# Performance work log

Measured on AMD Instinct MI355X. Metric: run time of the kernel, lower is better.

The kernel has to match this reference:

```python
import jax, jax.numpy as jnp
import numpy as np

B, S, V, E, H, MAX_OOVS = 32, 1024, 32000, 256, 512, 12
D2 = 2 * H + 100          # encoder feature dim after binary concat
IN = E + D2               # GRU input size


def setup_inputs() -> dict:
    key = jax.random.key(0)
    ks = jax.random.split(key, 18)
    sc = 0.02
    return {
        "input_idx": jax.random.randint(ks[0], (B,), 0, V),
        "encoded": jax.random.normal(ks[1], (B, S, 2 * H), jnp.float32),
        "encoded_idx": jax.random.randint(ks[2], (B, S), 0, V + MAX_OOVS),
        "prev_state": jax.random.normal(ks[3], (B, H), jnp.float32),
        "weighted": jax.random.normal(ks[4], (B, 1, D2), jnp.float32),
        "binary_vectors": jax.random.uniform(ks[5], (B, S, 1), jnp.float32),
        "order": 1,
        "embed_table": jax.random.normal(ks[6], (V, E), jnp.float32) * sc,
        "W_ih": jax.random.normal(ks[7], (3 * H, IN), jnp.float32) * sc,
        "b_ih": jax.random.normal(ks[8], (3 * H,), jnp.float32) * sc,
        "W_hh": jax.random.normal(ks[9], (3 * H, H), jnp.float32) * sc,
        "b_hh": jax.random.normal(ks[10], (3 * H,), jnp.float32) * sc,
        "Wo_w": jax.random.normal(ks[11], (V, H), jnp.float32) * sc,
        "Wo_b": jax.random.normal(ks[12], (V,), jnp.float32) * sc,
        "Wc_w": jax.random.normal(ks[13], (H, D2), jnp.float32) * sc,
        "Wc_b": jax.random.normal(ks[14], (H,), jnp.float32) * sc,
        "Ws_w": jax.random.normal(ks[15], (H, D2), jnp.float32) * sc,
        "Ws_b": jax.random.normal(ks[16], (H,), jnp.float32) * sc,
    }


def _gru_step(x, h, W_ih, b_ih, W_hh, b_hh):
    # torch nn.GRU single-step math
    gi = x @ W_ih.T + b_ih
    gh = h @ W_hh.T + b_hh
    i_r, i_z, i_n = jnp.split(gi, 3, axis=1)
    h_r, h_z, h_n = jnp.split(gh, 3, axis=1)
    r = jax.nn.sigmoid(i_r + h_r)
    z = jax.nn.sigmoid(i_z + h_z)
    n = jnp.tanh(i_n + r * h_n)
    return (1.0 - z) * n + z * h


def reference(input_idx, encoded, encoded_idx, prev_state, weighted,
              binary_vectors, order, embed_table, W_ih, b_ih, W_hh, b_hh,
              Wo_w, Wo_b, Wc_w, Wc_b, Ws_w, Ws_b):
    b, s = encoded.shape[0], encoded.shape[1]
    vocab = Wo_w.shape[0]
    # concat binary feature expanded to 100 channels -> (b, s, 2H+100)
    bin100 = jnp.broadcast_to(binary_vectors, (b, s, 100))
    enc = jnp.concatenate([encoded, bin100], axis=2)

    if order == 0:
        prev_state = enc[:, -1] @ Ws_w.T + Ws_b
        weighted = jnp.zeros((b, 1, enc.shape[2]), enc.dtype)

    emb = embed_table[input_idx][:, None, :]          # (b,1,E)
    x = jnp.concatenate([emb, weighted], axis=2)[:, 0]  # (b, IN)
    state = _gru_step(x, prev_state, W_ih, b_ih, W_hh, b_hh)  # (b,H)

    score_g = state @ Wo_w.T + Wo_b                   # (b, V)
    sc = jnp.tanh(enc @ Wc_w.T + Wc_b)                # (b, s, H)
    score_c = jnp.tanh(jnp.einsum('bsh,bh->bs', sc, state))
    score_c = score_c + jnp.where(encoded_idx == 0, -1000.0, 0.0).astype(score_c.dtype)

    probs = jax.nn.softmax(jnp.concatenate([score_g, score_c], axis=1), axis=1)
    prob_g = probs[:, :vocab]
    prob_c = probs[:, vocab:]
    prob_c_given = prob_c / jnp.sum(prob_c)           # faithful: scalar sum over all elems

    oovs = jnp.full((b, MAX_OOVS), 1e-4, probs.dtype)
    prob_g = jnp.concatenate([prob_g, oovs], axis=1)  # (b, V+OOV)

    # scatter-add copy probs into vocab space (same math as one_hot + bmm)
    rows = jnp.arange(b)[:, None]
    prob_c_to_g = jnp.zeros((b, vocab + MAX_OOVS), probs.dtype).at[rows, encoded_idx].add(prob_c)
    out = (prob_g + prob_c_to_g)[:, None, :]          # (b,1,V+OOV)

    idx_from = (encoded_idx == input_idx[:, None]).astype(probs.dtype)
    ssum = idx_from.sum(axis=1, keepdims=True)
    idx_from = jnp.where(ssum > 1, idx_from / ssum, idx_from)

    attn = prob_c_given * idx_from                    # (b, s)
    weighted_out = jnp.einsum('bs,bsd->bd', attn, enc)[:, None, :]
    return out, state, weighted_out
```

## Files before the change

kernel.cpp:

```cpp
#include <hip/hip_runtime.h>

#define B_   32
#define S_   1024
#define V_   32000
#define E_   256
#define H_   512
#define D2_  1124
#define IN_  1380
#define INP_ 1408
#define G3_  1536
#define NV_  33024
#define VO_  32012
#define NKT_ 36

typedef __bf16 bf16x8 __attribute__((ext_vector_type(8)));
typedef float  f32x4  __attribute__((ext_vector_type(4)));

static __device__ __forceinline__ unsigned short f2bf(float f) {
    union { float f; unsigned int u; } v; v.f = f;
    unsigned int u = v.u;
    unsigned int r = (u + 0x7FFFu + ((u >> 16) & 1u)) >> 16;
    return (unsigned short)r;
}

static __device__ __forceinline__ unsigned int pkbf(unsigned int a, unsigned int b) {
    return ((a + 0x8000u) >> 16) | ((b + 0x8000u) & 0xffff0000u);
}

__global__ void k_prep0(const int* order, const float* prev, const float* weighted,
                        const float* encoded, const float* bin,
                        const float* Ws_w, const float* Ws_b,
                        float* prev_eff, float* weff) {
    int b = blockIdx.x, t = threadIdx.x;
    if (order[0] != 0) {
        for (int i = t; i < H_;  i += 256) prev_eff[b * H_ + i] = prev[b * H_ + i];
        for (int i = t; i < D2_; i += 256) weff[b * D2_ + i] = weighted[b * D2_ + i];
    } else {
        for (int i = t; i < D2_; i += 256) weff[b * D2_ + i] = 0.0f;
        const float* encrow = encoded + ((size_t)(b * S_ + (S_ - 1))) * 1024;
        float bv = bin[b * S_ + (S_ - 1)];
        for (int h = t; h < H_; h += 256) {
            float acc = Ws_b[h];
            const float* wr = Ws_w + (size_t)h * D2_;
            for (int d = 0; d < 1024; d++) acc += encrow[d] * wr[d];
            for (int d = 1024; d < D2_; d++) acc += bv * wr[d];
            prev_eff[b * H_ + h] = acc;
        }
    }
}

__global__ void k_build_x(const int* input_idx, const float* embed, const float* weff, float* x) {
    int idx = blockIdx.x * 256 + threadIdx.x;
    int b = idx / INP_, d = idx % INP_;
    float v;
    if (d < E_)        v = embed[(size_t)input_idx[b] * E_ + d];
    else if (d < IN_)  v = weff[b * D2_ + (d - E_)];
    else               v = 0.0f;
    x[idx] = v;
}

__global__ void k_pack_wc(const float* Wc_w, unsigned short* bpack) {
    int idx = blockIdx.x * 256 + threadIdx.x;
    int j = idx & 7, lane = (idx >> 3) & 63, ht = (idx >> 9) & 31, kt = idx >> 14;
    int h = ht * 16 + (lane & 15);
    int k = kt * 32 + (lane >> 4) * 8 + j;
    float v = (k < D2_) ? Wc_w[(size_t)h * D2_ + k] : 0.0f;
    bpack[idx] = f2bf(v);
}

__global__ void k_gi(const float* x, const float* W_ih, const float* b_ih, float* gi) {
    extern __shared__ float smemF[];
    int t = threadIdx.x;
    int bh = blockIdx.x & 1;
    int hq = blockIdx.x >> 1;
    const float4* xg = (const float4*)(x + (size_t)bh * 16 * INP_);
    float4* xl4 = (float4*)smemF;
    for (int j = t; j < 16 * INP_ / 4; j += 256) xl4[j] = xg[j];
    __syncthreads();
    int w = t >> 6, l = t & 63;
    int h3 = hq * 4 + w;
    const float* wr = W_ih + (size_t)h3 * IN_;
    float4 wv[6];
#pragma unroll
    for (int i = 0; i < 6; i++) {
        int k = 4 * l + 256 * i;
        if (k + 3 < IN_) wv[i] = *(const float4*)(wr + k);
        else {
            float a0 = (k     < IN_) ? wr[k]     : 0.f;
            float a1 = (k + 1 < IN_) ? wr[k + 1] : 0.f;
            float a2 = (k + 2 < IN_) ? wr[k + 2] : 0.f;
            float a3 = (k + 3 < IN_) ? wr[k + 3] : 0.f;
            wv[i] = make_float4(a0, a1, a2, a3);
        }
    }
    float bias = b_ih[h3];
    for (int bb = 0; bb < 16; bb++) {
        const float4* xr = xl4 + bb * (INP_ / 4);
        float p = 0.f;
#pragma unroll
        for (int i = 0; i < 6; i++) {
            int k = 4 * l + 256 * i;
            if (k < INP_) {
                float4 xv = xr[l + 64 * i];
                p += wv[i].x * xv.x + wv[i].y * xv.y + wv[i].z * xv.z + wv[i].w * xv.w;
            }
        }
#pragma unroll
        for (int off = 32; off >= 1; off >>= 1) p += __shfl_xor(p, off, 64);
        if (l == 0) gi[(bh * 16 + bb) * G3_ + h3] = p + bias;
    }
}

__global__ void k_gh(const float* prev_eff, const float* W_hh, const float* b_hh, float* gh) {
    extern __shared__ float smemF[];
    int t = threadIdx.x;
    const float4* pg = (const float4*)prev_eff;
    float4* pl4 = (float4*)smemF;
    for (int j = t; j < B_ * H_ / 4; j += 256) pl4[j] = pg[j];
    __syncthreads();
    int w = t >> 6, l = t & 63;
    int h3 = blockIdx.x * 4 + w;
    const float* wr = W_hh + (size_t)h3 * H_;
    float4 w0 = *(const float4*)(wr + 4 * l);
    float4 w1 = *(const float4*)(wr + 256 + 4 * l);
    float bias = b_hh[h3];
    for (int bb = 0; bb < B_; bb++) {
        const float* pr = smemF + bb * H_;
        float4 s0 = *(const float4*)(pr + 4 * l);
        float4 s1 = *(const float4*)(pr + 256 + 4 * l);
        float p = w0.x * s0.x + w0.y * s0.y + w0.z * s0.z + w0.w * s0.w
                + w1.x * s1.x + w1.y * s1.y + w1.z * s1.z + w1.w * s1.w;
#pragma unroll
        for (int off = 32; off >= 1; off >>= 1) p += __shfl_xor(p, off, 64);
        if (l == 0) gh[bb * G3_ + h3] = p + bias;
    }
}

__global__ void k_gate(const float* gi, const float* gh, const float* prev_eff,
                       float* state, float* out_state) {
    int idx = blockIdx.x * 256 + threadIdx.x;
    int b = idx >> 9, h = idx & 511;
    float ir = gi[b * G3_ + h],           hr = gh[b * G3_ + h];
    float iz = gi[b * G3_ + H_ + h],      hz = gh[b * G3_ + H_ + h];
    float in_ = gi[b * G3_ + 2 * H_ + h], hn = gh[b * G3_ + 2 * H_ + h];
    float r = 1.0f / (1.0f + expf(-(ir + hr)));
    float z = 1.0f / (1.0f + expf(-(iz + hz)));
    float n = tanhf(in_ + r * hn);
    float st = (1.0f - z) * n + z * prev_eff[idx];
    state[idx] = st;
    out_state[idx] = st;
}

__global__ void __launch_bounds__(256) k_scoreg(const float* state, const float* Wo_w,
                                                const float* Wo_b, float* scores) {
    __shared__ unsigned short Abf[32 * 520];
    int t = threadIdx.x;
    {
        int m = t & 31, g = t >> 5;
        const float4* src = (const float4*)(state + m * 512 + g * 64);
        unsigned short* dst = &Abf[m * 520 + g * 64];
#pragma unroll
        for (int i = 0; i < 16; i++) {
            float4 v = src[i];
            ushort4 p; p.x = f2bf(v.x); p.y = f2bf(v.y); p.z = f2bf(v.z); p.w = f2bf(v.w);
            *(ushort4*)(dst + i * 4) = p;
        }
    }
    __syncthreads();
    int w = t >> 6, l = t & 63;
    int q = l >> 4, m16 = l & 15;
    int n = blockIdx.x * 64 + w * 16 + m16;
    const uint4* wrow = (const uint4*)(Wo_w + (size_t)n * 512 + q * 8);
    f32x4 acc0 = {0.f, 0.f, 0.f, 0.f}, acc1 = {0.f, 0.f, 0.f, 0.f};
#pragma unroll
    for (int kt = 0; kt < 16; kt++) {
        uint4 w0 = wrow[kt * 8];
        uint4 w1 = wrow[kt * 8 + 1];
        int4 pb;
        pb.x = (int)pkbf(w0.x, w0.y); pb.y = (int)pkbf(w0.z, w0.w);
        pb.z = (int)pkbf(w1.x, w1.y); pb.w = (int)pkbf(w1.z, w1.w);
        bf16x8 bv = *(bf16x8*)&pb;
        bf16x8 a0 = *(const bf16x8*)&Abf[m16 * 520 + kt * 32 + q * 8];
        bf16x8 a1 = *(const bf16x8*)&Abf[(16 + m16) * 520 + kt * 32 + q * 8];
        acc0 = __builtin_amdgcn_mfma_f32_16x16x32_bf16(a0, bv, acc0, 0, 0, 0);
        acc1 = __builtin_amdgcn_mfma_f32_16x16x32_bf16(a1, bv, acc1, 0, 0, 0);
    }
    float wb = Wo_b[n];
#pragma unroll
    for (int r = 0; r < 4; r++) {
        scores[(q * 4 + r) * NV_ + n]        = acc0[r] + wb;
        scores[(16 + q * 4 + r) * NV_ + n]   = acc1[r] + wb;
    }
}

__global__ void __launch_bounds__(512) k_sc(
    const float* encoded, const float* bin, const unsigned short* bpack,
    const float* Wc_b, const float* state, const int* enc_idx, float* scores) {
    __shared__ unsigned short Albf[64 * 40];
    __shared__ float partL[8][64];
    int t = threadIdx.x;
    int b = blockIdx.x >> 4;
    int s0 = (blockIdx.x & 15) * 64;
    int w = t >> 6, l = t & 63;
    int q = l >> 4, m = l & 15;

    f32x4 acc[4][4];
#pragma unroll
    for (int i = 0; i < 4; i++)
#pragma unroll
        for (int j2 = 0; j2 < 4; j2++) { acc[i][j2][0]=0.f; acc[i][j2][1]=0.f; acc[i][j2][2]=0.f; acc[i][j2][3]=0.f; }

    int s_l = t >> 3, k4 = (t & 7) * 4;
    const float* encbase = encoded + ((size_t)(b * S_ + s0 + s_l)) * 1024;
    float binv = bin[b * S_ + s0 + s_l];

    float4 nxt = *(const float4*)(encbase + k4);
    for (int kt = 0; kt < NKT_; kt++) {
        ushort4 pk;
        if (kt < 32) {
            pk.x = f2bf(nxt.x); pk.y = f2bf(nxt.y); pk.z = f2bf(nxt.z); pk.w = f2bf(nxt.w);
        } else {
            int k = kt * 32 + k4;
            pk.x = f2bf((k     < D2_) ? binv : 0.f);
            pk.y = f2bf((k + 1 < D2_) ? binv : 0.f);
            pk.z = f2bf((k + 2 < D2_) ? binv : 0.f);
            pk.w = f2bf((k + 3 < D2_) ? binv : 0.f);
        }
        *(ushort4*)&Albf[s_l * 40 + k4] = pk;
        __syncthreads();
        if (kt + 1 < 32)
            nxt = *(const float4*)(encbase + (kt + 1) * 32 + k4);

        bf16x8 av[4], bv[4];
#pragma unroll
        for (int st = 0; st < 4; st++)
            av[st] = *(const bf16x8*)&Albf[(st * 16 + m) * 40 + q * 8];
#pragma unroll
        for (int jj = 0; jj < 4; jj++)
            bv[jj] = *(const bf16x8*)&bpack[(((size_t)kt * 32 + (w * 4 + jj)) * 64 + l) * 8];
#pragma unroll
        for (int st = 0; st < 4; st++)
#pragma unroll
            for (int jj = 0; jj < 4; jj++)
                acc[st][jj] = __builtin_amdgcn_mfma_f32_16x16x32_bf16(av[st], bv[jj], acc[st][jj], 0, 0, 0);
        __syncthreads();
    }

    float hbias[4], hstate[4];
#pragma unroll
    for (int jj = 0; jj < 4; jj++) {
        int h = w * 64 + jj * 16 + m;
        hbias[jj]  = Wc_b[h];
        hstate[jj] = state[b * H_ + h];
    }
#pragma unroll
    for (int st = 0; st < 4; st++) {
#pragma unroll
        for (int r = 0; r < 4; r++) {
            float val = 0.f;
#pragma unroll
            for (int jj = 0; jj < 4; jj++)
                val += tanhf(acc[st][jj][r] + hbias[jj]) * hstate[jj];
            val += __shfl_xor(val, 1, 64);
            val += __shfl_xor(val, 2, 64);
            val += __shfl_xor(val, 4, 64);
            val += __shfl_xor(val, 8, 64);
            if (m == 0) partL[w][st * 16 + q * 4 + r] = val;
        }
    }
    __syncthreads();
    if (t < 64) {
        float tot = 0.f;
#pragma unroll
        for (int ww = 0; ww < 8; ww++) tot += partL[ww][t];
        int s = s0 + t;
        int ei = enc_idx[b * S_ + s];
        scores[b * NV_ + V_ + s] = tanhf(tot) + (ei == 0 ? -1000.0f : 0.0f);
    }
}

__global__ void k_exp(float* scores, float* partA, float* partC) {
    int blk = blockIdx.x;
    int b = blk >> 4, c = blk & 15;
    int t = threadIdx.x;
    float sa = 0.f, sc2 = 0.f;
    int base = b * NV_ + c * 2064;
    for (int i = t; i < 2064; i += 256) {
        float e = expf(scores[base + i]);
        scores[base + i] = e;
        sa += e;
        if (c * 2064 + i >= V_) sc2 += e;
    }
#pragma unroll
    for (int off = 32; off >= 1; off >>= 1) {
        sa  += __shfl_xor(sa, off, 64);
        sc2 += __shfl_xor(sc2, off, 64);
    }
    __shared__ float rA[4], rC[4];
    int w = t >> 6, l = t & 63;
    if (l == 0) { rA[w] = sa; rC[w] = sc2; }
    __syncthreads();
    if (t == 0) {
        partA[blk] = rA[0] + rA[1] + rA[2] + rA[3];
        partC[blk] = rC[0] + rC[1] + rC[2] + rC[3];
    }
}

__global__ void k_combine(const float* partA, const float* partC, float* rowinv, float* invgc,
                          int* cnt, int* list, const int* enc_idx, const int* input_idx) {
    __shared__ float rs[32], rc[32];
    int t = threadIdx.x;
    if (t < 32) {
        float a = 0.f, c = 0.f;
        for (int j = 0; j < 16; j++) { a += partA[t * 16 + j]; c += partC[t * 16 + j]; }
        rs[t] = a; rc[t] = c;
        rowinv[t] = 1.0f / a;
        cnt[t] = 0;
    }
    __syncthreads();
    if (t == 0) {
        float g = 0.f;
        for (int b = 0; b < 32; b++) g += rc[b] / rs[b];
        invgc[0] = 1.0f / g;
    }
    for (int i = t; i < B_ * S_; i += 512) {
        int b = i >> 10;
        if (enc_idx[i] == input_idx[b]) {
            int p = atomicAdd(&cnt[b], 1);
            list[b * S_ + p] = i & 1023;
        }
    }
}

__global__ void k_write(const float* scores, const float* rowinv, float* out, float* probc) {
    int idx = blockIdx.x * 256 + threadIdx.x;
    int b = idx / NV_, v = idx - b * NV_;
    float p = scores[idx] * rowinv[b];
    if (v < V_) out[b * VO_ + v] = p;
    else        probc[b * S_ + (v - V_)] = p;
}

__global__ void k_oov(float* out) {
    int idx = blockIdx.x * 256 + threadIdx.x;
    if (idx < B_ * 12) {
        int b = idx / 12, j = idx - b * 12;
        out[b * VO_ + V_ + j] = 0.0001f;
    }
}

__global__ void k_scatter(const float* probc, const int* enc_idx, float* out) {
    int idx = blockIdx.x * 256 + threadIdx.x;
    int b = idx >> 10;
    atomicAdd(&out[b * VO_ + enc_idx[idx]], probc[idx]);
}

__global__ void k_wo(const float* probc, const int* list, const int* cnt, const float* invgc,
                     const float* encoded, const float* bin, float* out2) {
    int b = blockIdx.x, t = threadIdx.x;
    __shared__ float aL[1024];
    __shared__ int   sL[1024];
    int n = cnt[b];
    float scale = invgc[0] * (n > 1 ? 1.0f / (float)n : 1.0f);
    for (int i = t; i < n; i += 256) {
        int s = list[b * S_ + i];
        sL[i] = s;
        aL[i] = probc[b * S_ + s] * scale;
    }
    __syncthreads();
    for (int d = t; d < D2_; d += 256) {
        float acc = 0.f;
        for (int i = 0; i < n; i++) {
            int s = sL[i];
            float ev = (d < 1024) ? encoded[((size_t)(b * S_ + s)) * 1024 + d] : bin[b * S_ + s];
            acc += aL[i] * ev;
        }
        out2[b * D2_ + d] = acc;
    }
}

extern "C" void kernel_launch(void* const* d_in, const int* in_sizes, int n_in,
                              void* d_out, int out_size, void* d_ws, size_t ws_size,
                              hipStream_t stream) {
    const int*   input_idx = (const int*)d_in[0];
    const float* encoded   = (const float*)d_in[1];
    const int*   enc_idx   = (const int*)d_in[2];
    const float* prev      = (const float*)d_in[3];
    const float* weighted  = (const float*)d_in[4];
    const float* bin       = (const float*)d_in[5];
    const int*   order     = (const int*)d_in[6];
    const float* embed     = (const float*)d_in[7];
    const float* W_ih      = (const float*)d_in[8];
    const float* b_ih      = (const float*)d_in[9];
    const float* W_hh      = (const float*)d_in[10];
    const float* b_hh      = (const float*)d_in[11];
    const float* Wo_w      = (const float*)d_in[12];
    const float* Wo_b      = (const float*)d_in[13];
    const float* Wc_w      = (const float*)d_in[14];
    const float* Wc_b      = (const float*)d_in[15];
    const float* Ws_w      = (const float*)d_in[16];
    const float* Ws_b      = (const float*)d_in[17];

    float* out  = (float*)d_out;
    float* out1 = out + B_ * VO_;
    float* out2 = out1 + B_ * H_;

    float* ws_f     = (float*)d_ws;
    float* w_state  = ws_f;
    float* w_prev   = ws_f + 16384;
    float* w_weff   = ws_f + 32768;
    float* w_x      = ws_f + 68736;
    float* w_gi     = ws_f + 113792;
    float* w_gh     = ws_f + 162944;
    float* w_scores = ws_f + 212096;
    float* w_probc  = ws_f + 1268864;
    float* w_partA  = ws_f + 1301632;
    float* w_partC  = ws_f + 1302144;
    float* w_rowinv = ws_f + 1302656;
    float* w_invgc  = ws_f + 1302688;
    int*   w_cnt    = (int*)(ws_f + 1302720);
    int*   w_list   = w_cnt + 32;
    unsigned short* w_bpack = (unsigned short*)((char*)d_ws + 5342080);

    k_prep0<<<32, 256, 0, stream>>>(order, prev, weighted, encoded, bin, Ws_w, Ws_b, w_prev, w_weff);
    k_build_x<<<176, 256, 0, stream>>>(input_idx, embed, w_weff, w_x);
    k_pack_wc<<<2304, 256, 0, stream>>>(Wc_w, w_bpack);
    k_gi<<<768, 256, 16 * INP_ * sizeof(float), stream>>>(w_x, W_ih, b_ih, w_gi);
    k_gh<<<384, 256, B_ * H_ * sizeof(float), stream>>>(w_prev, W_hh, b_hh, w_gh);
    k_gate<<<64, 256, 0, stream>>>(w_gi, w_gh, w_prev, w_state, out1);
    k_scoreg<<<500, 256, 0, stream>>>(w_state, Wo_w, Wo_b, w_scores);
    k_sc<<<512, 512, 0, stream>>>(encoded, bin, w_bpack, Wc_b, w_state, enc_idx, w_scores);
    k_exp<<<512, 256, 0, stream>>>(w_scores, w_partA, w_partC);
    k_combine<<<1, 512, 0, stream>>>(w_partA, w_partC, w_rowinv, w_invgc, w_cnt, w_list, enc_idx, input_idx);
    k_write<<<4128, 256, 0, stream>>>(w_scores, w_rowinv, out, w_probc);
    k_oov<<<2, 256, 0, stream>>>(out);
    k_scatter<<<128, 256, 0, stream>>>(w_probc, enc_idx, out);
    k_wo<<<32, 256, 0, stream>>>(w_probc, w_list, w_cnt, w_invgc, encoded, bin, out2);
}
```

Before: 440.2 us.

## Restructure copy-score GEMM with double-buffered swizzled LDS and split-H atomics

```diff
diff --git a/kernel.cpp b/kernel.cpp
--- a/kernel.cpp
+++ b/kernel.cpp
@@ -9,7 +9,6 @@
 #define IN_  1380
 #define INP_ 1408
 #define G3_  1536
-#define NV_  33024
 #define VO_  32012
 #define NKT_ 36
 
@@ -25,6 +24,28 @@
 
 static __device__ __forceinline__ unsigned int pkbf(unsigned int a, unsigned int b) {
     return ((a + 0x8000u) >> 16) | ((b + 0x8000u) & 0xffff0000u);
+}
+
+static __device__ __forceinline__ uint4 pack4(uint4 a, uint4 b) {
+    uint4 o;
+    o.x = pkbf(a.x, a.y); o.y = pkbf(a.z, a.w);
+    o.z = pkbf(b.x, b.y); o.w = pkbf(b.z, b.w);
+    return o;
+}
+
+static __device__ __forceinline__ uint4 pack_bin(unsigned int binu, int kbase) {
+    unsigned int x[8];
+#pragma unroll
+    for (int j = 0; j < 8; j++) x[j] = (kbase + j < D2_) ? binu : 0u;
+    uint4 o;
+    o.x = pkbf(x[0], x[1]); o.y = pkbf(x[2], x[3]);
+    o.z = pkbf(x[4], x[5]); o.w = pkbf(x[6], x[7]);
+    return o;
+}
+
+static __device__ __forceinline__ float tanh_fast(float x) {
+    float e = __builtin_amdgcn_exp2f(x * 2.8853901817f);
+    return 1.0f - 2.0f * __builtin_amdgcn_rcpf(e + 1.0f);
 }
 
 __global__ void k_prep0(const int* order, const float* prev, const float* weighted,
@@ -152,7 +173,7 @@
 }
 
 __global__ void __launch_bounds__(256) k_scoreg(const float* state, const float* Wo_w,
-                                                const float* Wo_b, float* scores) {
+                                                const float* Wo_b, float* scoreg) {
     __shared__ unsigned short Abf[32 * 520];
     int t = threadIdx.x;
     {
@@ -188,121 +209,147 @@
     float wb = Wo_b[n];
 #pragma unroll
     for (int r = 0; r < 4; r++) {
-        scores[(q * 4 + r) * NV_ + n]        = acc0[r] + wb;
-        scores[(16 + q * 4 + r) * NV_ + n]   = acc1[r] + wb;
-    }
-}
-
-__global__ void __launch_bounds__(512) k_sc(
+        scoreg[(q * 4 + r) * V_ + n]        = acc0[r] + wb;
+        scoreg[(16 + q * 4 + r) * V_ + n]   = acc1[r] + wb;
+    }
+}
+
+__global__ void __launch_bounds__(256) k_sc(
     const float* encoded, const float* bin, const unsigned short* bpack,
-    const float* Wc_b, const float* state, const int* enc_idx, float* scores) {
-    __shared__ unsigned short Albf[64 * 40];
-    __shared__ float partL[8][64];
-    int t = threadIdx.x;
-    int b = blockIdx.x >> 4;
-    int s0 = (blockIdx.x & 15) * 64;
+    const float* Wc_b, const float* state, float* scorec) {
+    __shared__ unsigned short Abuf[2][4096];
+    __shared__ float partL[4][128];
+    int t = threadIdx.x;
+    int b  = blockIdx.x >> 4;
+    int s0 = ((blockIdx.x >> 1) & 7) << 7;
+    int hh = blockIdx.x & 1;
     int w = t >> 6, l = t & 63;
     int q = l >> 4, m = l & 15;
 
-    f32x4 acc[4][4];
-#pragma unroll
-    for (int i = 0; i < 4; i++)
-#pragma unroll
-        for (int j2 = 0; j2 < 4; j2++) { acc[i][j2][0]=0.f; acc[i][j2][1]=0.f; acc[i][j2][2]=0.f; acc[i][j2][3]=0.f; }
-
-    int s_l = t >> 3, k4 = (t & 7) * 4;
-    const float* encbase = encoded + ((size_t)(b * S_ + s0 + s_l)) * 1024;
-    float binv = bin[b * S_ + s0 + s_l];
-
-    float4 nxt = *(const float4*)(encbase + k4);
+    int r   = t >> 1;
+    int cq0 = t & 1;
+    int cq1 = cq0 + 2;
+    const uint4* encp = (const uint4*)(encoded + ((size_t)(b * S_ + s0 + r)) * 1024);
+    unsigned int binu = __float_as_uint(bin[b * S_ + s0 + r]);
+    int wro0 = r * 32 + ((cq0 ^ (r & 3)) << 3);
+    int wro1 = r * 32 + ((cq1 ^ (r & 3)) << 3);
+
+    f32x4 acc[8][4];
+#pragma unroll
+    for (int i = 0; i < 8; i++)
+#pragma unroll
+        for (int j = 0; j < 4; j++) { acc[i][j][0]=0.f; acc[i][j][1]=0.f; acc[i][j][2]=0.f; acc[i][j][3]=0.f; }
+
+    {
+        uint4 a0 = encp[cq0 * 2], a1 = encp[cq0 * 2 + 1];
+        uint4 b0 = encp[cq1 * 2], b1 = encp[cq1 * 2 + 1];
+        *(uint4*)&Abuf[0][wro0] = pack4(a0, a1);
+        *(uint4*)&Abuf[0][wro1] = pack4(b0, b1);
+    }
+    const unsigned short* bvbase = bpack + ((size_t)((hh * 16 + w * 4) * 64 + l)) * 8;
+    __syncthreads();
+    bf16x8 bv[4];
+#pragma unroll
+    for (int jj = 0; jj < 4; jj++) bv[jj] = *(const bf16x8*)(bvbase + jj * 512);
+
+#pragma unroll 2
     for (int kt = 0; kt < NKT_; kt++) {
-        ushort4 pk;
-        if (kt < 32) {
-            pk.x = f2bf(nxt.x); pk.y = f2bf(nxt.y); pk.z = f2bf(nxt.z); pk.w = f2bf(nxt.w);
-        } else {
-            int k = kt * 32 + k4;
-            pk.x = f2bf((k     < D2_) ? binv : 0.f);
-            pk.y = f2bf((k + 1 < D2_) ? binv : 0.f);
-            pk.z = f2bf((k + 2 < D2_) ? binv : 0.f);
-            pk.w = f2bf((k + 3 < D2_) ? binv : 0.f);
-        }
-        *(ushort4*)&Albf[s_l * 40 + k4] = pk;
+        int cur = kt & 1;
+        uint4 na0, na1, nb0, nb1;
+        if (kt + 1 < 32) {
+            na0 = encp[(kt + 1) * 8 + cq0 * 2]; na1 = encp[(kt + 1) * 8 + cq0 * 2 + 1];
+            nb0 = encp[(kt + 1) * 8 + cq1 * 2]; nb1 = encp[(kt + 1) * 8 + cq1 * 2 + 1];
+        }
+        bf16x8 bvn[4];
+        if (kt + 1 < NKT_) {
+#pragma unroll
+            for (int jj = 0; jj < 4; jj++)
+                bvn[jj] = *(const bf16x8*)(bvbase + (size_t)(kt + 1) * 16384 + jj * 512);
+        }
+#pragma unroll
+        for (int st = 0; st < 8; st++) {
+            bf16x8 a = *(const bf16x8*)&Abuf[cur][(st * 16 + m) * 32 + ((q ^ (m & 3)) << 3)];
+#pragma unroll
+            for (int jj = 0; jj < 4; jj++)
+                acc[st][jj] = __builtin_amdgcn_mfma_f32_16x16x32_bf16(a, bv[jj], acc[st][jj], 0, 0, 0);
+        }
+        if (kt + 1 < NKT_) {
+            uint4 p0, p1;
+            if (kt + 1 < 32) { p0 = pack4(na0, na1); p1 = pack4(nb0, nb1); }
+            else {
+                p0 = pack_bin(binu, (kt + 1) * 32 + cq0 * 8);
+                p1 = pack_bin(binu, (kt + 1) * 32 + cq1 * 8);
+            }
+            *(uint4*)&Abuf[cur ^ 1][wro0] = p0;
+            *(uint4*)&Abuf[cur ^ 1][wro1] = p1;
+        }
         __syncthreads();
-        if (kt + 1 < 32)
-            nxt = *(const float4*)(encbase + (kt + 1) * 32 + k4);
-
-        bf16x8 av[4], bv[4];
-#pragma unroll
-        for (int st = 0; st < 4; st++)
-            av[st] = *(const bf16x8*)&Albf[(st * 16 + m) * 40 + q * 8];
-#pragma unroll
-        for (int jj = 0; jj < 4; jj++)
-            bv[jj] = *(const bf16x8*)&bpack[(((size_t)kt * 32 + (w * 4 + jj)) * 64 + l) * 8];
-#pragma unroll
-        for (int st = 0; st < 4; st++)
+#pragma unroll
+        for (int jj = 0; jj < 4; jj++) bv[jj] = bvn[jj];
+    }
+
+    float hb[4], hs[4];
+#pragma unroll
+    for (int jj = 0; jj < 4; jj++) {
+        int h = (hh * 16 + w * 4 + jj) * 16 + m;
+        hb[jj] = Wc_b[h];
+        hs[jj] = state[b * H_ + h];
+    }
+#pragma unroll
+    for (int st = 0; st < 8; st++) {
+#pragma unroll
+        for (int rr = 0; rr < 4; rr++) {
+            float val = 0.f;
 #pragma unroll
             for (int jj = 0; jj < 4; jj++)
-                acc[st][jj] = __builtin_amdgcn_mfma_f32_16x16x32_bf16(av[st], bv[jj], acc[st][jj], 0, 0, 0);
-        __syncthreads();
-    }
-
-    float hbias[4], hstate[4];
-#pragma unroll
-    for (int jj = 0; jj < 4; jj++) {
-        int h = w * 64 + jj * 16 + m;
-        hbias[jj]  = Wc_b[h];
-        hstate[jj] = state[b * H_ + h];
-    }
-#pragma unroll
-    for (int st = 0; st < 4; st++) {
-#pragma unroll
-        for (int r = 0; r < 4; r++) {
-            float val = 0.f;
-#pragma unroll
-            for (int jj = 0; jj < 4; jj++)
-                val += tanhf(acc[st][jj][r] + hbias[jj]) * hstate[jj];
+                val += tanh_fast(acc[st][jj][rr] + hb[jj]) * hs[jj];
             val += __shfl_xor(val, 1, 64);
             val += __shfl_xor(val, 2, 64);
             val += __shfl_xor(val, 4, 64);
             val += __shfl_xor(val, 8, 64);
-            if (m == 0) partL[w][st * 16 + q * 4 + r] = val;
-        }
-    }
-    __syncthreads();
-    if (t < 64) {
-        float tot = 0.f;
-#pragma unroll
-        for (int ww = 0; ww < 8; ww++) tot += partL[ww][t];
-        int s = s0 + t;
-        int ei = enc_idx[b * S_ + s];
-        scores[b * NV_ + V_ + s] = tanhf(tot) + (ei == 0 ? -1000.0f : 0.0f);
-    }
-}
-
-__global__ void k_exp(float* scores, float* partA, float* partC) {
+            if (m == 0) partL[w][st * 16 + q * 4 + rr] = val;
+        }
+    }
+    __syncthreads();
+    if (t < 128) {
+        float tot = partL[0][t] + partL[1][t] + partL[2][t] + partL[3][t];
+        atomicAdd(&scorec[b * 1024 + s0 + t], tot);
+    }
+}
+
+__global__ void k_exp(float* scoreg, float* scorec, const int* enc_idx,
+                      float* partA, float* partC) {
     int blk = blockIdx.x;
-    int b = blk >> 4, c = blk & 15;
-    int t = threadIdx.x;
-    float sa = 0.f, sc2 = 0.f;
-    int base = b * NV_ + c * 2064;
-    for (int i = t; i < 2064; i += 256) {
-        float e = expf(scores[base + i]);
-        scores[base + i] = e;
-        sa += e;
-        if (c * 2064 + i >= V_) sc2 += e;
-    }
-#pragma unroll
-    for (int off = 32; off >= 1; off >>= 1) {
-        sa  += __shfl_xor(sa, off, 64);
-        sc2 += __shfl_xor(sc2, off, 64);
-    }
-    __shared__ float rA[4], rC[4];
+    int b = blk / 17, c = blk % 17;
+    int t = threadIdx.x;
+    float sa = 0.f;
+    if (c < 16) {
+        int base = b * V_ + c * 2000;
+        for (int i = t; i < 2000; i += 256) {
+            float e = __expf(scoreg[base + i]);
+            scoreg[base + i] = e;
+            sa += e;
+        }
+    } else {
+        int base = b * 1024;
+        for (int i = t; i < 1024; i += 256) {
+            float v = scorec[base + i];
+            float s = tanh_fast(v) + (enc_idx[base + i] == 0 ? -1000.0f : 0.0f);
+            float e = __expf(s);
+            scorec[base + i] = e;
+            sa += e;
+        }
+    }
+#pragma unroll
+    for (int off = 32; off >= 1; off >>= 1) sa += __shfl_xor(sa, off, 64);
+    __shared__ float rA[4];
     int w = t >> 6, l = t & 63;
-    if (l == 0) { rA[w] = sa; rC[w] = sc2; }
+    if (l == 0) rA[w] = sa;
     __syncthreads();
     if (t == 0) {
-        partA[blk] = rA[0] + rA[1] + rA[2] + rA[3];
-        partC[blk] = rC[0] + rC[1] + rC[2] + rC[3];
+        float tot = rA[0] + rA[1] + rA[2] + rA[3];
+        partA[blk] = tot;
+        if (c == 16) partC[b] = tot;
     }
 }
 
@@ -311,9 +358,9 @@
     __shared__ float rs[32], rc[32];
     int t = threadIdx.x;
     if (t < 32) {
-        float a = 0.f, c = 0.f;
-        for (int j = 0; j < 16; j++) { a += partA[t * 16 + j]; c += partC[t * 16 + j]; }
-        rs[t] = a; rc[t] = c;
+        float a = 0.f;
+        for (int j = 0; j < 17; j++) a += partA[t * 17 + j];
+        rs[t] = a; rc[t] = partC[t];
         rowinv[t] = 1.0f / a;
         cnt[t] = 0;
     }
@@ -332,19 +379,22 @@
     }
 }
 
-__global__ void k_write(const float* scores, const float* rowinv, float* out, float* probc) {
+__global__ void k_write(const float* scoreg, const float* scorec, const float* rowinv,
+                        float* out, float* probc) {
     int idx = blockIdx.x * 256 + threadIdx.x;
-    int b = idx / NV_, v = idx - b * NV_;
-    float p = scores[idx] * rowinv[b];
-    if (v < V_) out[b * VO_ + v] = p;
-    else        probc[b * S_ + (v - V_)] = p;
-}
-
-__global__ void k_oov(float* out) {
-    int idx = blockIdx.x * 256 + threadIdx.x;
-    if (idx < B_ * 12) {
-        int b = idx / 12, j = idx - b * 12;
-        out[b * VO_ + V_ + j] = 0.0001f;
+    if (idx < B_ * V_) {
+        int b = idx / V_, v = idx - b * V_;
+        out[b * VO_ + v] = scoreg[idx] * rowinv[b];
+    } else if (idx < B_ * V_ + B_ * S_) {
+        int j = idx - B_ * V_;
+        int b = j >> 10;
+        probc[j] = scorec[j] * rowinv[b];
+    } else {
+        int j = idx - B_ * V_ - B_ * S_;
+        if (j < B_ * 12) {
+            int b = j / 12;
+            out[b * VO_ + V_ + (j - b * 12)] = 0.0001f;
+        }
     }
 }
 
@@ -411,15 +461,16 @@
     float* w_x      = ws_f + 68736;
     float* w_gi     = ws_f + 113792;
     float* w_gh     = ws_f + 162944;
-    float* w_scores = ws_f + 212096;
+    float* w_scoreg = ws_f + 212096;
+    float* w_scorec = ws_f + 1236096;
     float* w_probc  = ws_f + 1268864;
     float* w_partA  = ws_f + 1301632;
-    float* w_partC  = ws_f + 1302144;
-    float* w_rowinv = ws_f + 1302656;
-    float* w_invgc  = ws_f + 1302688;
-    int*   w_cnt    = (int*)(ws_f + 1302720);
+    float* w_partC  = ws_f + 1302176;
+    float* w_rowinv = ws_f + 1302208;
+    float* w_invgc  = ws_f + 1302240;
+    int*   w_cnt    = (int*)(ws_f + 1302248);
     int*   w_list   = w_cnt + 32;
-    unsigned short* w_bpack = (unsigned short*)((char*)d_ws + 5342080);
+    unsigned short* w_bpack = (unsigned short*)(ws_f + 1335048);
 
     k_prep0<<<32, 256, 0, stream>>>(order, prev, weighted, encoded, bin, Ws_w, Ws_b, w_prev, w_weff);
     k_build_x<<<176, 256, 0, stream>>>(input_idx, embed, w_weff, w_x);
@@ -427,12 +478,12 @@
     k_gi<<<768, 256, 16 * INP_ * sizeof(float), stream>>>(w_x, W_ih, b_ih, w_gi);
     k_gh<<<384, 256, B_ * H_ * sizeof(float), stream>>>(w_prev, W_hh, b_hh, w_gh);
     k_gate<<<64, 256, 0, stream>>>(w_gi, w_gh, w_prev, w_state, out1);
-    k_scoreg<<<500, 256, 0, stream>>>(w_state, Wo_w, Wo_b, w_scores);
-    k_sc<<<512, 512, 0, stream>>>(encoded, bin, w_bpack, Wc_b, w_state, enc_idx, w_scores);
-    k_exp<<<512, 256, 0, stream>>>(w_scores, w_partA, w_partC);
+    hipMemsetAsync(w_scorec, 0, B_ * S_ * sizeof(float), stream);
+    k_scoreg<<<500, 256, 0, stream>>>(w_state, Wo_w, Wo_b, w_scoreg);
+    k_sc<<<512, 256, 0, stream>>>(encoded, bin, w_bpack, Wc_b, w_state, w_scorec);
+    k_exp<<<544, 256, 0, stream>>>(w_scoreg, w_scorec, enc_idx, w_partA, w_partC);
     k_combine<<<1, 512, 0, stream>>>(w_partA, w_partC, w_rowinv, w_invgc, w_cnt, w_list, enc_idx, input_idx);
-    k_write<<<4128, 256, 0, stream>>>(w_scores, w_rowinv, out, w_probc);
-    k_oov<<<2, 256, 0, stream>>>(out);
+    k_write<<<4130, 256, 0, stream>>>(w_scoreg, w_scorec, w_rowinv, out, w_probc);
     k_scatter<<<128, 256, 0, stream>>>(w_probc, enc_idx, out);
     k_wo<<<32, 256, 0, stream>>>(w_probc, w_list, w_cnt, w_invgc, encoded, bin, out2);
 }
```

New measurement: 466.7 us. 1.06x slower.
